# Kernel tuning notes

Measured on AMD Instinct MI355X. Metric: run time of the kernel, lower is better.

## Reference

```python
import jax, jax.numpy as jnp
import numpy as np

L, H, Z, B, SRC, K = 2, 1024, 256, 128, 64, 48
IN = Z + 1 + H  # z_i (+) k (+) attn


def _init(key, shape, fan_in):
    return jax.random.normal(key, shape, jnp.float32) / np.sqrt(fan_in)


def setup_inputs() -> dict:
    key = jax.random.key(0)
    ks = jax.random.split(key, 24)
    inp = {
        "h0": jax.random.normal(ks[0], (L, B, H), jnp.float32),
        "c0": jax.random.normal(ks[1], (L, B, H), jnp.float32),
        "context": jax.random.normal(ks[2], (B, SRC, H), jnp.float32),
        "z_0": jax.random.normal(ks[3], (B, Z), jnp.float32),
        "k": jax.random.randint(ks[4], (B, 1), 1, K + 1, jnp.int32),
        "eps": jax.random.normal(ks[5], (K, B, Z), jnp.float32),
        # StackedLSTM layer 0 (input IN) and layer 1 (input H)
        "W_ih0": _init(ks[6], (4 * H, IN), IN), "W_hh0": _init(ks[7], (4 * H, H), H),
        "b_ih0": jnp.zeros((4 * H,), jnp.float32), "b_hh0": jnp.zeros((4 * H,), jnp.float32),
        "W_ih1": _init(ks[8], (4 * H, H), H), "W_hh1": _init(ks[9], (4 * H, H), H),
        "b_ih1": jnp.zeros((4 * H,), jnp.float32), "b_hh1": jnp.zeros((4 * H,), jnp.float32),
        # GlobalAttentionLatent (Luong general)
        "attn_W_in": _init(ks[10], (H, H), H), "attn_W_out": _init(ks[11], (H, 2 * H), 2 * H),
        # GeneratorLatent
        "mu_W": _init(ks[12], (Z, H), H), "mu_b": jnp.zeros((Z,), jnp.float32),
        "sigma_W": _init(ks[13], (Z, H), H), "sigma_b": jnp.zeros((Z,), jnp.float32),
    }
    return inp


def _lstm_cell(x, h, c, W_ih, W_hh, b_ih, b_hh):
    gates = x @ W_ih.T + b_ih + h @ W_hh.T + b_hh
    i, f, g, o = jnp.split(gates, 4, axis=1)
    c_new = jax.nn.sigmoid(f) * c + jax.nn.sigmoid(i) * jnp.tanh(g)
    h_new = jax.nn.sigmoid(o) * jnp.tanh(c_new)
    return h_new, c_new


def _attend(q, context, W_in, W_out):
    # q: [B,H], context: [B,S,H] -> [B,H]
    scores = jnp.einsum('bsh,bh->bs', context, q @ W_in.T)
    align = jax.nn.softmax(scores, axis=1)
    weighted = jnp.einsum('bs,bsh->bh', align, context)
    return jnp.tanh(jnp.concatenate([weighted, q], axis=1) @ W_out.T)


def _forward(h0, c0, context, z_0, k, eps,
             W_ih0, W_hh0, b_ih0, b_hh0, W_ih1, W_hh1, b_ih1, b_hh1,
             attn_W_in, attn_W_out, mu_W, mu_b, sigma_W, sigma_b):
    k_max = eps.shape[0]
    k_f = k.astype(jnp.float32)  # [B,1]
    attn0 = _attend(c0[-1], context, attn_W_in, attn_W_out)

    def step(carry, inp):
        z_i, attn_o, h, c = carry
        i, eps_i = inp
        x = jnp.concatenate([z_i, k_f, attn_o], axis=1)  # [B, Z+1+H]
        h0n, c0n = _lstm_cell(x, h[0], c[0], W_ih0, W_hh0, b_ih0, b_hh0)
        h1n, c1n = _lstm_cell(h0n, h[1], c[1], W_ih1, W_hh1, b_ih1, b_hh1)
        h_new = jnp.stack([h0n, h1n])
        c_new = jnp.stack([c0n, c1n])
        frozen = (i >= k_f).astype(h_new.dtype)[None]  # [1,B,1]
        h_new = frozen * h + (1.0 - frozen) * h_new
        c_new = frozen * c + (1.0 - frozen) * c_new
        output = h1n  # rnn output before freezing, as in torch
        mu_i = output @ mu_W.T + mu_b
        sig_i = output @ sigma_W.T + sigma_b
        z_next = mu_i + jnp.exp(sig_i) * eps_i
        attn_new = _attend(output, context, attn_W_in, attn_W_out)
        return (z_next, attn_new, h_new, c_new), (z_next, mu_i, sig_i)

    steps = jnp.arange(k_max, dtype=jnp.float32)
    (_, _, h_f, c_f), (z, mu, sigma) = jax.lax.scan(
        step, (z_0, attn0, h0, c0), (steps, eps))
    valid = (steps[:, None] < k_f[:, 0][None, :])[:, :, None]  # [K,B,1]
    z = jnp.where(valid, z, 0.0)
    mu = jnp.where(valid, mu, 0.0)
    sigma = jnp.where(valid, sigma, 0.0)
    return (z.transpose(1, 0, 2), mu.transpose(1, 0, 2), sigma.transpose(1, 0, 2), h_f, c_f)


def reference(h0, c0, context, z_0, k, eps,
              W_ih0, W_hh0, b_ih0, b_hh0, W_ih1, W_hh1, b_ih1, b_hh1,
              attn_W_in, attn_W_out, mu_W, mu_b, sigma_W, sigma_b):
    return _forward(h0, c0, context, z_0, k, eps,
                    W_ih0, W_hh0, b_ih0, b_hh0, W_ih1, W_hh1, b_ih1, b_hh1,
                    attn_W_in, attn_W_out, mu_W, mu_b, sigma_W, sigma_b)
```

## Files before the change

kernel.cpp:

```cpp
#include <hip/hip_runtime.h>
#include <hip/hip_bf16.h>

#define L_ 2
#define H_ 1024
#define Z_ 256
#define B_ 128
#define SRC_ 64
#define K_ 48
#define BH_ (B_ * H_)
#define BZ_ (B_ * Z_)
#define BKZ_ ((size_t)B_ * K_ * Z_)
#define KA_ 2304
#define KB_ 2048

typedef unsigned short u16;
typedef __attribute__((ext_vector_type(8))) short short8;
typedef __attribute__((ext_vector_type(4))) float f32x4;

__device__ __align__(16) u16 g_Wc0[4096 * KA_];
__device__ __align__(16) u16 g_Wc1[4096 * KB_];
__device__ __align__(16) u16 g_Wmq[512 * 1024];
__device__ __align__(16) u16 g_Woutb[1024 * 2048];
__device__ __align__(16) u16 g_WinT[1024 * 1024];
__device__ __align__(16) u16 g_ctxb[8192 * 1024];
__device__ __align__(16) u16 g_ctxW[8192 * 1024];
__device__ __align__(16) u16 g_ctxWin[8192 * 1024];
__device__ __align__(16) u16 g_XA[2][B_ * KA_];
__device__ __align__(16) u16 g_XB[2][B_ * KB_];
__device__ __align__(16) u16 g_XC[B_ * H_];
__device__ float g_pb0[4096], g_pb1[4096], g_pbmq[512], g_wk0[4096];
__device__ float g_cs0[BH_], g_cs1[BH_], g_align[B_ * SRC_];
__device__ float g_cred[B_ * H_];
__device__ int g_perm[B_], g_inv[B_], g_kr[B_], g_Mact[K_];

__device__ __forceinline__ float sigm(float x) { return 1.0f / (1.0f + expf(-x)); }
__device__ __forceinline__ u16 f2b(float f) {
    union { float f; unsigned u; } x; x.f = f;
    unsigned r = x.u + 0x7fffu + ((x.u >> 16) & 1u);
    return (u16)(r >> 16);
}
__device__ __forceinline__ float b2f(u16 s) {
    union { unsigned u; float f; } x; x.u = ((unsigned)s) << 16;
    return x.f;
}

__global__ void k_sort(const int* __restrict__ kvec) {
    __shared__ int ks[B_];
    int t = threadIdx.x;
    if (t < B_) ks[t] = kvec[t];
    __syncthreads();
    if (t < B_) {
        int kb = ks[t], rank = 0;
        for (int j = 0; j < B_; ++j) { int kj = ks[j]; rank += (kj > kb) || (kj == kb && j < t); }
        g_perm[rank] = t; g_inv[t] = rank; g_kr[rank] = kb;
    }
    if (t < K_) { int c = 0; for (int j = 0; j < B_; ++j) c += (ks[j] > t); g_Mact[t] = c; }
}

__global__ void k_zero(float* __restrict__ out) {
    size_t n = 3 * BKZ_;
    for (size_t i = (size_t)blockIdx.x * 256 + threadIdx.x; i < n; i += (size_t)gridDim.x * 256)
        out[i] = 0.f;
}

__global__ void prep_wc0(const float* __restrict__ Wih, const float* __restrict__ Whh,
                         const float* __restrict__ bih, const float* __restrict__ bhh) {
    int n = blockIdx.x;
    int h = n >> 2, g = n & 3, r = g * 1024 + h;
    u16* row = g_Wc0 + (size_t)n * KA_;
    for (int j = threadIdx.x; j < KA_; j += 256) {
        float v = (j < 256) ? Wih[(size_t)r * 1281 + j]
                : (j < 1280) ? Wih[(size_t)r * 1281 + j + 1]
                             : Whh[(size_t)r * 1024 + (j - 1280)];
        row[j] = f2b(v);
    }
    if (threadIdx.x == 0) {
        g_wk0[n] = Wih[(size_t)r * 1281 + 256];
        g_pb0[n] = bih[r] + bhh[r];
    }
}

__global__ void prep_wc1(const float* __restrict__ Wih, const float* __restrict__ Whh,
                         const float* __restrict__ bih, const float* __restrict__ bhh) {
    int n = blockIdx.x;
    int h = n >> 2, g = n & 3, r = g * 1024 + h;
    u16* row = g_Wc1 + (size_t)n * KB_;
    for (int j = threadIdx.x; j < KB_; j += 256) {
        float v = (j < 1024) ? Wih[(size_t)r * 1024 + j] : Whh[(size_t)r * 1024 + (j - 1024)];
        row[j] = f2b(v);
    }
    if (threadIdx.x == 0) g_pb1[n] = bih[r] + bhh[r];
}

__global__ void prep_wmq(const float* __restrict__ muW, const float* __restrict__ mub,
                         const float* __restrict__ sgW, const float* __restrict__ sgb) {
    int n = blockIdx.x;
    int z = n >> 1, sel = n & 1;
    const float* src = sel ? sgW : muW;
    u16* row = g_Wmq + (size_t)n * 1024;
    for (int j = threadIdx.x; j < 1024; j += 256) row[j] = f2b(src[(size_t)z * 1024 + j]);
    if (threadIdx.x == 0) g_pbmq[n] = sel ? sgb[z] : mub[z];
}

__global__ void prep_copy(const float* __restrict__ in, u16* __restrict__ out, int n) {
    for (int i = blockIdx.x * 256 + threadIdx.x; i < n; i += gridDim.x * 256)
        out[i] = f2b(in[i]);
}

__global__ void prep_winT(const float* __restrict__ Win) {
    __shared__ float t[32][33];
    int bx = blockIdx.x * 32, by = blockIdx.y * 32;
    int tx = threadIdx.x & 31, ty0 = threadIdx.x >> 5;
    for (int it = 0; it < 4; ++it) {
        int ty = ty0 + it * 8;
        t[ty][tx] = Win[(size_t)(by + ty) * 1024 + bx + tx];
    }
    __syncthreads();
    for (int it = 0; it < 4; ++it) {
        int ty = ty0 + it * 8;
        g_WinT[(size_t)(bx + ty) * 1024 + by + tx] = f2b(t[tx][ty]);
    }
}

template <int K>
__device__ __forceinline__ void mmq(const u16* __restrict__ A, int sA,
                                    const u16* __restrict__ W, int sW,
                                    int m0, int n0, int w, int lane, f32x4& acc) {
    constexpr int KQ = K / 4;
    const int quad = lane >> 4, l16 = lane & 15;
    const u16* pa = A + (size_t)(m0 + l16) * sA + w * KQ + quad * 8;
    const u16* pw = W + (size_t)(n0 + l16) * sW + w * KQ + quad * 8;
#pragma unroll 4
    for (int k0 = 0; k0 < KQ; k0 += 32) {
        short8 a = *(const short8*)(const void*)(pa + k0);
        short8 b = *(const short8*)(const void*)(pw + k0);
        acc = __builtin_amdgcn_mfma_f32_16x16x32_bf16(a, b, acc, 0, 0, 0);
    }
}

__device__ __forceinline__ void stage_q(float* sm, int w, int lane, const f32x4& acc) {
    int quad = lane >> 4, l16 = lane & 15;
#pragma unroll
    for (int r = 0; r < 4; ++r) sm[w * 272 + (quad * 4 + r) * 17 + l16] = acc[r];
}

template <int K>
__device__ __forceinline__ void mm32(const u16* __restrict__ A, int sA,
                                     const u16* __restrict__ W, int sW,
                                     int m0, int n0, int w, int lane, f32x4 acc[2][2]) {
    constexpr int KQ = K / 4;
    const int quad = lane >> 4, l16 = lane & 15;
    const u16* pa0 = A + (size_t)(m0 + l16) * sA + w * KQ + quad * 8;
    const u16* pa1 = pa0 + (size_t)16 * sA;
    const u16* pb0 = W + (size_t)(n0 + l16) * sW + w * KQ + quad * 8;
    const u16* pb1 = pb0 + (size_t)16 * sW;
#pragma unroll 2
    for (int k0 = 0; k0 < KQ; k0 += 32) {
        short8 a0 = *(const short8*)(const void*)(pa0 + k0);
        short8 a1 = *(const short8*)(const void*)(pa1 + k0);
        short8 b0 = *(const short8*)(const void*)(pb0 + k0);
        short8 b1 = *(const short8*)(const void*)(pb1 + k0);
        acc[0][0] = __builtin_amdgcn_mfma_f32_16x16x32_bf16(a0, b0, acc[0][0], 0, 0, 0);
        acc[0][1] = __builtin_amdgcn_mfma_f32_16x16x32_bf16(a0, b1, acc[0][1], 0, 0, 0);
        acc[1][0] = __builtin_amdgcn_mfma_f32_16x16x32_bf16(a1, b0, acc[1][0], 0, 0, 0);
        acc[1][1] = __builtin_amdgcn_mfma_f32_16x16x32_bf16(a1, b1, acc[1][1], 0, 0, 0);
    }
}

template <int LAYER>
__global__ __launch_bounds__(256) void k_lstm(int step) {
    constexpr int K = (LAYER == 0) ? KA_ : KB_;
    const int p = step & 1;
    const u16* A = (LAYER == 0) ? g_XA[p] : g_XB[p];
    const u16* W = (LAYER == 0) ? g_Wc0 : g_Wc1;
    const float* pb = (LAYER == 0) ? g_pb0 : g_pb1;
    float* cs = (LAYER == 0) ? g_cs0 : g_cs1;
    const u16* stOld = (LAYER == 0) ? (g_XA[p] + 1280) : (g_XB[p] + 1024);
    u16* stNew = (LAYER == 0) ? (g_XA[1 - p] + 1280) : (g_XB[1 - p] + 1024);
    u16* hout = (LAYER == 0) ? g_XB[p] : g_XC;
    const int hoStride = (LAYER == 0) ? KB_ : 1024;

    const int tid = threadIdx.x, w = tid >> 6, lane = tid & 63;
    const int xcd = blockIdx.x & 7, loc = blockIdx.x >> 3;
    const int mt = loc & 3, nl = loc >> 2;
    const int m0 = mt * 32;
    const int n0 = (xcd * 16 + nl) * 32;
    const int Mact = g_Mact[step];

    if (m0 >= Mact) {
        const int r = m0 + (tid & 31), hg = (n0 >> 2) + (tid >> 5);
        stNew[(size_t)r * K + hg] = stOld[(size_t)r * K + hg];
        return;
    }

    __shared__ float smf[4 * 32 * 33];
    f32x4 acc[2][2] = {};
    mm32<K>(A, K, W, K, m0, n0, w, lane, acc);
    const int quad = lane >> 4, l16 = lane & 15;
#pragma unroll
    for (int i = 0; i < 2; ++i)
#pragma unroll
        for (int j = 0; j < 2; ++j)
#pragma unroll
            for (int r = 0; r < 4; ++r)
                smf[(w * 32 + i * 16 + quad * 4 + r) * 33 + j * 16 + l16] = acc[i][j][r];
    __syncthreads();
    const int bl = tid & 31, hl = tid >> 5;
    const int r = m0 + bl;
    float g[4];
#pragma unroll
    for (int gg = 0; gg < 4; ++gg) {
        int c = hl * 4 + gg;
        float s = smf[bl * 33 + c] + smf[(32 + bl) * 33 + c] +
                  smf[(64 + bl) * 33 + c] + smf[(96 + bl) * 33 + c];
        g[gg] = s + pb[n0 + c];
    }
    const int kr = g_kr[r];
    if (LAYER == 0) {
        float kf = (float)kr;
#pragma unroll
        for (int gg = 0; gg < 4; ++gg) g[gg] += kf * g_wk0[n0 + hl * 4 + gg];
    }
    const int hg = (n0 >> 2) + hl;
    float cold = cs[r * 1024 + hg];
    float cn = sigm(g[1]) * cold + sigm(g[0]) * tanhf(g[2]);
    float hn = sigm(g[3]) * tanhf(cn);
    hout[(size_t)r * hoStride + hg] = f2b(hn);
    if (step < kr) {
        stNew[(size_t)r * K + hg] = f2b(hn);
        cs[r * 1024 + hg] = cn;
    } else {
        stNew[(size_t)r * K + hg] = stOld[(size_t)r * K + hg];
    }
}

__global__ __launch_bounds__(256) void k_mix(const float* __restrict__ eps,
                                             float* __restrict__ out, int step,
                                             int do_mu, int do_sc) {
    __shared__ float sm[1344];
    const int tid = threadIdx.x;
    const int Mact = g_Mact[step];
    if (blockIdx.x < 256) {
        if (!do_mu) return;
        const int w = tid >> 6, lane = tid & 63;
        const int xcd = blockIdx.x & 7, loc = blockIdx.x >> 3;
        const int mt = loc & 7, nl = loc >> 3;
        const int m0 = mt * 16;
        const int n0 = (xcd * 4 + nl) * 16;
        if (m0 >= Mact) return;
        f32x4 acc = {0.f, 0.f, 0.f, 0.f};
        mmq<1024>(g_XC, 1024, g_Wmq, 1024, m0, n0, w, lane, acc);
        stage_q(sm, w, lane, acc);
        __syncthreads();
        if (tid < 128) {
            int bl = tid & 15, zl = tid >> 4;
            int r = m0 + bl;
            int c0 = 2 * zl, c1 = 2 * zl + 1;
            float mu = sm[bl * 17 + c0] + sm[272 + bl * 17 + c0] +
                       sm[544 + bl * 17 + c0] + sm[816 + bl * 17 + c0] + g_pbmq[n0 + c0];
            float sg = sm[bl * 17 + c1] + sm[272 + bl * 17 + c1] +
                       sm[544 + bl * 17 + c1] + sm[816 + bl * 17 + c1] + g_pbmq[n0 + c1];
            int zg = (n0 >> 1) + zl;
            int b = g_perm[r];
            float e = eps[((size_t)step * B_ + b) * Z_ + zg];
            float zn = mu + expf(sg) * e;
            g_XA[(step + 1) & 1][(size_t)r * KA_ + zg] = f2b(zn);
            bool valid = step < g_kr[r];
            size_t o = ((size_t)b * K_ + step) * Z_ + zg;
            out[o] = valid ? zn : 0.f;
            out[BKZ_ + o] = valid ? mu : 0.f;
            out[2 * BKZ_ + o] = valid ? sg : 0.f;
        }
    } else if (blockIdx.x < 384) {
        if (!do_sc) return;
        const int r = blockIdx.x - 256;
        if (r >= Mact) return;
        float* qf = sm;
        float* parts = sm + 1024;
        for (int i = tid; i < 1024; i += 256) qf[i] = b2f(g_XC[r * 1024 + i]);
        __syncthreads();
        int s = tid >> 2, part = tid & 3;
        const int b = g_perm[r];
        const u16* row = g_ctxWin + ((size_t)(b * SRC_ + s)) * 1024 + part * 256;
        float pacc = 0.f;
        for (int j = 0; j < 256; j += 8) {
            short8 v = *(const short8*)(const void*)(row + j);
#pragma unroll
            for (int t = 0; t < 8; ++t) pacc += qf[part * 256 + j + t] * b2f(((u16*)&v)[t]);
        }
        parts[s * 4 + part] = pacc;
        __syncthreads();
        if (tid < 64) {
            float v = parts[tid * 4] + parts[tid * 4 + 1] + parts[tid * 4 + 2] + parts[tid * 4 + 3];
            float mx = v;
            for (int o = 32; o; o >>= 1) mx = fmaxf(mx, __shfl_xor(mx, o, 64));
            float e = expf(v - mx), sum = e;
            for (int o = 32; o; o >>= 1) sum += __shfl_xor(sum, o, 64);
            g_align[r * SRC_ + tid] = e / sum;
        }
    } else {
        if (!do_sc) return;
        const int w = tid >> 6, lane = tid & 63;
        const int t = blockIdx.x - 384;
        const int xcd = t & 7, loc = t >> 3;
        const int mt = loc & 7, nl = loc >> 3;
        const int m0 = mt * 16;
        const int n0 = (xcd * 8 + nl) * 16;
        if (m0 >= Mact) return;
        f32x4 acc = {0.f, 0.f, 0.f, 0.f};
        mmq<1024>(g_XC, 1024, g_Woutb + 1024, 2048, m0, n0, w, lane, acc);
        stage_q(sm, w, lane, acc);
        __syncthreads();
        int bl = tid >> 4, hc = tid & 15;
        float cred = sm[bl * 17 + hc] + sm[272 + bl * 17 + hc] +
                     sm[544 + bl * 17 + hc] + sm[816 + bl * 17 + hc];
        g_cred[(size_t)(m0 + bl) * 1024 + n0 + hc] = cred;
    }
}

__global__ __launch_bounds__(256) void k_contract(int dp, int step) {
    __shared__ float sm[16 * SRC_];
    const int tid = threadIdx.x;
    const int xcd = blockIdx.x & 7, loc = blockIdx.x >> 3;
    const int mt = loc & 7, nl = loc >> 3;
    const int m0 = mt * 16;
    const int n0 = (xcd * 8 + nl) * 16;
    if (m0 >= g_Mact[step]) return;
    for (int i = tid; i < 16 * SRC_; i += 256)
        sm[i] = g_align[(m0 + (i >> 6)) * SRC_ + (i & 63)];
    __syncthreads();
    int bl = tid >> 4, hc = tid & 15;
    int r = m0 + bl;
    const int b = g_perm[r];
    const u16* base = g_ctxW + ((size_t)b * SRC_) * 1024 + n0 + hc;
    float a = g_cred[(size_t)r * 1024 + n0 + hc];
#pragma unroll 8
    for (int s = 0; s < SRC_; ++s) a += sm[bl * 64 + s] * b2f(base[(size_t)s * 1024]);
    g_XA[dp][(size_t)r * KA_ + 256 + n0 + hc] = f2b(tanhf(a));
}

__global__ void k_init(const float* __restrict__ h0, const float* __restrict__ c0,
                       const float* __restrict__ z0) {
    int i = blockIdx.x * 256 + threadIdx.x;
    int b = i >> 10, h = i & 1023;
    int r = g_inv[b];
    g_XA[0][(size_t)r * KA_ + 1280 + h] = f2b(h0[i]);
    g_XB[0][(size_t)r * KB_ + 1024 + h] = f2b(h0[BH_ + i]);
    g_XC[r * 1024 + h] = f2b(c0[BH_ + i]);
    g_cs0[r * 1024 + h] = c0[i];
    g_cs1[r * 1024 + h] = c0[BH_ + i];
    if (i < BZ_) {
        int bb = i >> 8, z = i & 255;
        g_XA[0][(size_t)g_inv[bb] * KA_ + z] = f2b(z0[i]);
    }
}

__global__ void k_final(float* __restrict__ out) {
    int i = blockIdx.x * 256 + threadIdx.x;
    int b = i >> 10, h = i & 1023;
    int r = g_inv[b];
    float* hf = out + (size_t)3 * BKZ_;
    float* cf = hf + 2 * BH_;
    hf[i] = b2f(g_XA[0][(size_t)r * KA_ + 1280 + h]);
    hf[BH_ + i] = b2f(g_XB[0][(size_t)r * KB_ + 1024 + h]);
    cf[i] = g_cs0[r * 1024 + h];
    cf[BH_ + i] = g_cs1[r * 1024 + h];
}

__global__ __launch_bounds__(256) void k_gemm_prep(const u16* __restrict__ A, int sA,
                                                   const u16* __restrict__ W, int sW,
                                                   u16* __restrict__ Out, int sO) {
    const int tid = threadIdx.x, w = tid >> 6, lane = tid & 63;
    const int quad = lane >> 4, l16 = lane & 15;
    const int xcd = blockIdx.x & 7, loc = blockIdx.x >> 3;
    const int n0 = (xcd * 2 + (loc & 1)) * 64;
    const int mb = (loc >> 1) * 128 + w * 32;
    f32x4 acc[2][4] = {};
    const u16* pa0 = A + (size_t)(mb + l16) * sA + quad * 8;
    const u16* pa1 = pa0 + (size_t)16 * sA;
    const u16* pw = W + (size_t)(n0 + l16) * sW + quad * 8;
#pragma unroll 2
    for (int k0 = 0; k0 < 1024; k0 += 32) {
        short8 a0 = *(const short8*)(const void*)(pa0 + k0);
        short8 a1 = *(const short8*)(const void*)(pa1 + k0);
#pragma unroll
        for (int j = 0; j < 4; ++j) {
            short8 b = *(const short8*)(const void*)(pw + (size_t)j * 16 * sW + k0);
            acc[0][j] = __builtin_amdgcn_mfma_f32_16x16x32_bf16(a0, b, acc[0][j], 0, 0, 0);
            acc[1][j] = __builtin_amdgcn_mfma_f32_16x16x32_bf16(a1, b, acc[1][j], 0, 0, 0);
        }
    }
#pragma unroll
    for (int i = 0; i < 2; ++i)
#pragma unroll
        for (int j = 0; j < 4; ++j)
#pragma unroll
            for (int r = 0; r < 4; ++r)
                Out[(size_t)(mb + i * 16 + quad * 4 + r) * sO + n0 + j * 16 + l16] =
                    f2b(acc[i][j][r]);
}

extern "C" void kernel_launch(void* const* d_in, const int* in_sizes, int n_in,
                              void* d_out, int out_size, void* d_ws, size_t ws_size,
                              hipStream_t stream) {
    (void)in_sizes; (void)n_in; (void)out_size; (void)d_ws; (void)ws_size;
    const float* h0 = (const float*)d_in[0];
    const float* c0 = (const float*)d_in[1];
    const float* ctx = (const float*)d_in[2];
    const float* z0 = (const float*)d_in[3];
    const int* kvec = (const int*)d_in[4];
    const float* eps = (const float*)d_in[5];
    const float* Wih0 = (const float*)d_in[6];
    const float* Whh0 = (const float*)d_in[7];
    const float* bih0 = (const float*)d_in[8];
    const float* bhh0 = (const float*)d_in[9];
    const float* Wih1 = (const float*)d_in[10];
    const float* Whh1 = (const float*)d_in[11];
    const float* bih1 = (const float*)d_in[12];
    const float* bhh1 = (const float*)d_in[13];
    const float* Win = (const float*)d_in[14];
    const float* Wout = (const float*)d_in[15];
    const float* muW = (const float*)d_in[16];
    const float* mub = (const float*)d_in[17];
    const float* sgW = (const float*)d_in[18];
    const float* sgb = (const float*)d_in[19];
    float* out = (float*)d_out;

    dim3 blk(256);
    k_sort<<<1, 128, 0, stream>>>(kvec);
    k_zero<<<2048, blk, 0, stream>>>(out);
    prep_wc0<<<4096, blk, 0, stream>>>(Wih0, Whh0, bih0, bhh0);
    prep_wc1<<<4096, blk, 0, stream>>>(Wih1, Whh1, bih1, bhh1);
    prep_wmq<<<512, blk, 0, stream>>>(muW, mub, sgW, sgb);
    {
        u16* woutb; hipGetSymbolAddress((void**)&woutb, HIP_SYMBOL(g_Woutb));
        u16* ctxb; hipGetSymbolAddress((void**)&ctxb, HIP_SYMBOL(g_ctxb));
        u16* winT; hipGetSymbolAddress((void**)&winT, HIP_SYMBOL(g_WinT));
        u16* ctxW; hipGetSymbolAddress((void**)&ctxW, HIP_SYMBOL(g_ctxW));
        u16* ctxWin; hipGetSymbolAddress((void**)&ctxWin, HIP_SYMBOL(g_ctxWin));
        prep_copy<<<2048, blk, 0, stream>>>(Wout, woutb, 1024 * 2048);
        prep_copy<<<8192, blk, 0, stream>>>(ctx, ctxb, 8192 * 1024);
        prep_winT<<<dim3(32, 32), blk, 0, stream>>>(Win);
        k_gemm_prep<<<1024, blk, 0, stream>>>(ctxb, 1024, woutb, 2048, ctxW, 1024);
        k_gemm_prep<<<1024, blk, 0, stream>>>(ctxb, 1024, winT, 1024, ctxWin, 1024);
    }
    k_init<<<BH_ / 256, blk, 0, stream>>>(h0, c0, z0);
    k_mix<<<896, blk, 0, stream>>>(eps, out, 0, 0, 1);
    k_contract<<<512, blk, 0, stream>>>(0, 0);

    for (int i = 0; i < K_; ++i) {
        k_lstm<0><<<512, blk, 0, stream>>>(i);
        k_lstm<1><<<512, blk, 0, stream>>>(i);
        const int more = (i + 1 < K_) ? 1 : 0;
        k_mix<<<896, blk, 0, stream>>>(eps, out, i, 1, more);
        if (more) k_contract<<<512, blk, 0, stream>>>((i + 1) & 1, i);
    }
    k_final<<<BH_ / 256, blk, 0, stream>>>(out);
}
```

Measured before the change: 3.213 ms.

## Fuse per-step recurrent kernels into one persistent kernel with grid barriers

Replaces the roughly 190 per-step kernel launches (two LSTM layers, mix, contract) with a single persistent kernel of 1024 blocks that moves between phases through a hierarchical atomic grid barrier, with per-XCD counters feeding a global counter. The aim is to remove launch overhead and inter-kernel gaps across the 48 sequential steps. It also merges the two precompute GEMMs into one launch with smaller per-warp tiles and raises the unroll factor in the LSTM matmul loop. The change relies on all 1024 blocks being co-resident; if they are not, the barrier deadlocks. Idle blocks in phases that use fewer blocks also spin at the barrier.

```diff
diff --git a/kernel.cpp b/kernel.cpp
--- a/kernel.cpp
+++ b/kernel.cpp
@@ -12,6 +12,8 @@
 #define BKZ_ ((size_t)B_ * K_ * Z_)
 #define KA_ 2304
 #define KB_ 2048
+#define NBLK_ 1024
+#define GRP_ (NBLK_ / 8)
 
 typedef unsigned short u16;
 typedef __attribute__((ext_vector_type(8))) short short8;
@@ -33,6 +35,9 @@
 __device__ float g_cred[B_ * H_];
 __device__ int g_perm[B_], g_inv[B_], g_kr[B_], g_Mact[K_];
 
+__device__ __align__(128) unsigned g_bar_x[8][32];
+__device__ __align__(128) unsigned g_bar_g;
+
 __device__ __forceinline__ float sigm(float x) { return 1.0f / (1.0f + expf(-x)); }
 __device__ __forceinline__ u16 f2b(float f) {
     union { float f; unsigned u; } x; x.f = f;
@@ -42,6 +47,22 @@
 __device__ __forceinline__ float b2f(u16 s) {
     union { unsigned u; float f; } x; x.u = ((unsigned)s) << 16;
     return x.f;
+}
+
+__device__ __forceinline__ void gsync(int bid, int bar) {
+    __syncthreads();
+    if (threadIdx.x == 0) {
+        __builtin_amdgcn_fence(__ATOMIC_RELEASE, "agent");
+        unsigned v = __hip_atomic_fetch_add(&g_bar_x[bid & 7][0], 1u,
+                                            __ATOMIC_RELAXED, __HIP_MEMORY_SCOPE_AGENT);
+        if (v == (unsigned)(bar * GRP_ + (GRP_ - 1)))
+            __hip_atomic_fetch_add(&g_bar_g, 1u, __ATOMIC_RELAXED, __HIP_MEMORY_SCOPE_AGENT);
+        while (__hip_atomic_load(&g_bar_g, __ATOMIC_RELAXED, __HIP_MEMORY_SCOPE_AGENT)
+               < (unsigned)(bar * 8 + 8))
+            __builtin_amdgcn_s_sleep(8);
+        __builtin_amdgcn_fence(__ATOMIC_ACQUIRE, "agent");
+    }
+    __syncthreads();
 }
 
 __global__ void k_sort(const int* __restrict__ kvec) {
@@ -154,7 +175,7 @@
     const u16* pa1 = pa0 + (size_t)16 * sA;
     const u16* pb0 = W + (size_t)(n0 + l16) * sW + w * KQ + quad * 8;
     const u16* pb1 = pb0 + (size_t)16 * sW;
-#pragma unroll 2
+#pragma unroll 4
     for (int k0 = 0; k0 < KQ; k0 += 32) {
         short8 a0 = *(const short8*)(const void*)(pa0 + k0);
         short8 a1 = *(const short8*)(const void*)(pa1 + k0);
@@ -168,7 +189,9 @@
 }
 
 template <int LAYER>
-__global__ __launch_bounds__(256) void k_lstm(int step) {
+__device__ __forceinline__ void lstm_phase(int bid, int tid, int w, int lane,
+                                           float* smf, int step) {
+    if (bid >= 512) return;
     constexpr int K = (LAYER == 0) ? KA_ : KB_;
     const int p = step & 1;
     const u16* A = (LAYER == 0) ? g_XA[p] : g_XB[p];
@@ -180,8 +203,7 @@
     u16* hout = (LAYER == 0) ? g_XB[p] : g_XC;
     const int hoStride = (LAYER == 0) ? KB_ : 1024;
 
-    const int tid = threadIdx.x, w = tid >> 6, lane = tid & 63;
-    const int xcd = blockIdx.x & 7, loc = blockIdx.x >> 3;
+    const int xcd = bid & 7, loc = bid >> 3;
     const int mt = loc & 3, nl = loc >> 2;
     const int m0 = mt * 32;
     const int n0 = (xcd * 16 + nl) * 32;
@@ -193,7 +215,6 @@
         return;
     }
 
-    __shared__ float smf[4 * 32 * 33];
     f32x4 acc[2][2] = {};
     mm32<K>(A, K, W, K, m0, n0, w, lane, acc);
     const int quad = lane >> 4, l16 = lane & 15;
@@ -234,16 +255,14 @@
     }
 }
 
-__global__ __launch_bounds__(256) void k_mix(const float* __restrict__ eps,
-                                             float* __restrict__ out, int step,
-                                             int do_mu, int do_sc) {
-    __shared__ float sm[1344];
-    const int tid = threadIdx.x;
+__device__ __forceinline__ void mix_phase(int bid, int tid, int w, int lane, float* sm,
+                                          const float* __restrict__ eps,
+                                          float* __restrict__ out,
+                                          int step, bool musig, bool sc) {
     const int Mact = g_Mact[step];
-    if (blockIdx.x < 256) {
-        if (!do_mu) return;
-        const int w = tid >> 6, lane = tid & 63;
-        const int xcd = blockIdx.x & 7, loc = blockIdx.x >> 3;
+    if (bid < 256) {
+        if (!musig) return;
+        const int xcd = bid & 7, loc = bid >> 3;
         const int mt = loc & 7, nl = loc >> 3;
         const int m0 = mt * 16;
         const int n0 = (xcd * 4 + nl) * 16;
@@ -271,9 +290,9 @@
             out[BKZ_ + o] = valid ? mu : 0.f;
             out[2 * BKZ_ + o] = valid ? sg : 0.f;
         }
-    } else if (blockIdx.x < 384) {
-        if (!do_sc) return;
-        const int r = blockIdx.x - 256;
+    } else if (bid < 384) {
+        if (!sc) return;
+        const int r = bid - 256;
         if (r >= Mact) return;
         float* qf = sm;
         float* parts = sm + 1024;
@@ -298,10 +317,9 @@
             for (int o = 32; o; o >>= 1) sum += __shfl_xor(sum, o, 64);
             g_align[r * SRC_ + tid] = e / sum;
         }
-    } else {
-        if (!do_sc) return;
-        const int w = tid >> 6, lane = tid & 63;
-        const int t = blockIdx.x - 384;
+    } else if (bid < 896) {
+        if (!sc) return;
+        const int t = bid - 384;
         const int xcd = t & 7, loc = t >> 3;
         const int mt = loc & 7, nl = loc >> 3;
         const int m0 = mt * 16;
@@ -318,10 +336,9 @@
     }
 }
 
-__global__ __launch_bounds__(256) void k_contract(int dp, int step) {
-    __shared__ float sm[16 * SRC_];
-    const int tid = threadIdx.x;
-    const int xcd = blockIdx.x & 7, loc = blockIdx.x >> 3;
+__device__ __forceinline__ void contract_phase(int bid, int tid, float* sm, int dp, int step) {
+    if (bid >= 512) return;
+    const int xcd = bid & 7, loc = bid >> 3;
     const int mt = loc & 7, nl = loc >> 3;
     const int m0 = mt * 16;
     const int n0 = (xcd * 8 + nl) * 16;
@@ -339,6 +356,34 @@
     g_XA[dp][(size_t)r * KA_ + 256 + n0 + hc] = f2b(tanhf(a));
 }
 
+__global__ __launch_bounds__(256, 4) void k_persist(const float* __restrict__ eps,
+                                                    float* __restrict__ out) {
+    const int bid = blockIdx.x;
+    const int tid = threadIdx.x;
+    const int w = tid >> 6, lane = tid & 63;
+    __shared__ float smf[4 * 32 * 33];
+    int bar = 0;
+
+    mix_phase(bid, tid, w, lane, smf, eps, out, 0, false, true);
+    gsync(bid, bar); ++bar;
+    contract_phase(bid, tid, smf, 0, 0);
+    gsync(bid, bar); ++bar;
+
+    for (int i = 0; i < K_; ++i) {
+        lstm_phase<0>(bid, tid, w, lane, smf, i);
+        gsync(bid, bar); ++bar;
+        lstm_phase<1>(bid, tid, w, lane, smf, i);
+        gsync(bid, bar); ++bar;
+        const bool more = (i + 1) < K_;
+        mix_phase(bid, tid, w, lane, smf, eps, out, i, true, more);
+        if (more) {
+            gsync(bid, bar); ++bar;
+            contract_phase(bid, tid, smf, (i + 1) & 1, i);
+            gsync(bid, bar); ++bar;
+        }
+    }
+}
+
 __global__ void k_init(const float* __restrict__ h0, const float* __restrict__ c0,
                        const float* __restrict__ z0) {
     int i = blockIdx.x * 256 + threadIdx.x;
@@ -353,6 +398,10 @@
         int bb = i >> 8, z = i & 255;
         g_XA[0][(size_t)g_inv[bb] * KA_ + z] = f2b(z0[i]);
     }
+    if (blockIdx.x == 0 && threadIdx.x == 0) {
+        g_bar_g = 0;
+        for (int x = 0; x < 8; ++x) g_bar_x[x][0] = 0;
+    }
 }
 
 __global__ void k_final(float* __restrict__ out) {
@@ -367,36 +416,45 @@
     cf[BH_ + i] = g_cs1[r * 1024 + h];
 }
 
-__global__ __launch_bounds__(256) void k_gemm_prep(const u16* __restrict__ A, int sA,
-                                                   const u16* __restrict__ W, int sW,
-                                                   u16* __restrict__ Out, int sO) {
+__global__ __launch_bounds__(256) void k_prep2(const u16* __restrict__ A,
+                                               const u16* __restrict__ W0,
+                                               const u16* __restrict__ W1,
+                                               u16* __restrict__ O0,
+                                               u16* __restrict__ O1) {
     const int tid = threadIdx.x, w = tid >> 6, lane = tid & 63;
     const int quad = lane >> 4, l16 = lane & 15;
+    const int wm = w >> 1, wn = w & 1;
     const int xcd = blockIdx.x & 7, loc = blockIdx.x >> 3;
-    const int n0 = (xcd * 2 + (loc & 1)) * 64;
-    const int mb = (loc >> 1) * 128 + w * 32;
-    f32x4 acc[2][4] = {};
-    const u16* pa0 = A + (size_t)(mb + l16) * sA + quad * 8;
-    const u16* pa1 = pa0 + (size_t)16 * sA;
-    const u16* pw = W + (size_t)(n0 + l16) * sW + quad * 8;
-#pragma unroll 2
+    const int nsub = loc & 3, mt = loc >> 2;
+    const bool sel = nsub >= 2;
+    const u16* W = sel ? W1 : W0;
+    const int sW = sel ? 1024 : 2048;
+    u16* Out = sel ? O1 : O0;
+    const int n0 = (xcd * 2 + (nsub & 1)) * 64 + wn * 32;
+    const int mb = mt * 64 + wm * 32;
+    f32x4 acc[2][2] = {};
+    const u16* pa0 = A + (size_t)(mb + l16) * 1024 + quad * 8;
+    const u16* pa1 = pa0 + (size_t)16 * 1024;
+    const u16* pb0 = W + (size_t)(n0 + l16) * sW + quad * 8;
+    const u16* pb1 = pb0 + (size_t)16 * sW;
+#pragma unroll 4
     for (int k0 = 0; k0 < 1024; k0 += 32) {
         short8 a0 = *(const short8*)(const void*)(pa0 + k0);
         short8 a1 = *(const short8*)(const void*)(pa1 + k0);
-#pragma unroll
-        for (int j = 0; j < 4; ++j) {
-            short8 b = *(const short8*)(const void*)(pw + (size_t)j * 16 * sW + k0);
-            acc[0][j] = __builtin_amdgcn_mfma_f32_16x16x32_bf16(a0, b, acc[0][j], 0, 0, 0);
-            acc[1][j] = __builtin_amdgcn_mfma_f32_16x16x32_bf16(a1, b, acc[1][j], 0, 0, 0);
-        }
+        short8 b0 = *(const short8*)(const void*)(pb0 + k0);
+        short8 b1 = *(const short8*)(const void*)(pb1 + k0);
+        acc[0][0] = __builtin_amdgcn_mfma_f32_16x16x32_bf16(a0, b0, acc[0][0], 0, 0, 0);
+        acc[0][1] = __builtin_amdgcn_mfma_f32_16x16x32_bf16(a0, b1, acc[0][1], 0, 0, 0);
+        acc[1][0] = __builtin_amdgcn_mfma_f32_16x16x32_bf16(a1, b0, acc[1][0], 0, 0, 0);
+        acc[1][1] = __builtin_amdgcn_mfma_f32_16x16x32_bf16(a1, b1, acc[1][1], 0, 0, 0);
     }
 #pragma unroll
     for (int i = 0; i < 2; ++i)
 #pragma unroll
-        for (int j = 0; j < 4; ++j)
+        for (int j = 0; j < 2; ++j)
 #pragma unroll
             for (int r = 0; r < 4; ++r)
-                Out[(size_t)(mb + i * 16 + quad * 4 + r) * sO + n0 + j * 16 + l16] =
+                Out[(size_t)(mb + i * 16 + quad * 4 + r) * 1024 + n0 + j * 16 + l16] =
                     f2b(acc[i][j][r]);
 }
 
@@ -441,19 +499,9 @@
         prep_copy<<<2048, blk, 0, stream>>>(Wout, woutb, 1024 * 2048);
         prep_copy<<<8192, blk, 0, stream>>>(ctx, ctxb, 8192 * 1024);
         prep_winT<<<dim3(32, 32), blk, 0, stream>>>(Win);
-        k_gemm_prep<<<1024, blk, 0, stream>>>(ctxb, 1024, woutb, 2048, ctxW, 1024);
-        k_gemm_prep<<<1024, blk, 0, stream>>>(ctxb, 1024, winT, 1024, ctxWin, 1024);
+        k_prep2<<<4096, blk, 0, stream>>>(ctxb, woutb, winT, ctxW, ctxWin);
     }
     k_init<<<BH_ / 256, blk, 0, stream>>>(h0, c0, z0);
-    k_mix<<<896, blk, 0, stream>>>(eps, out, 0, 0, 1);
-    k_contract<<<512, blk, 0, stream>>>(0, 0);
-
-    for (int i = 0; i < K_; ++i) {
-        k_lstm<0><<<512, blk, 0, stream>>>(i);
-        k_lstm<1><<<512, blk, 0, stream>>>(i);
-        const int more = (i + 1 < K_) ? 1 : 0;
-        k_mix<<<896, blk, 0, stream>>>(eps, out, i, 1, more);
-        if (more) k_contract<<<512, blk, 0, stream>>>((i + 1) & 1, i);
-    }
+    k_persist<<<NBLK_, blk, 0, stream>>>(eps, out);
     k_final<<<BH_ / 256, blk, 0, stream>>>(out);
 }
```

After: 9.096 ms. 183% more time.

## Fuse per-step kernels into one persistent kernel with custom grid barrier

Applied to the files above, without the earlier changes.

Replaces the roughly 190 per-step kernel launches of the recurrent loop with a single persistent kernel of 1024 blocks. The kernel runs the LSTM, mix and contract phases in sequence, separated by a software grid barrier built on flag arrays and cache-bypassing loads and stores. Double-buffered state arrays are expanded to one buffer per step, so no phase ever overwrites data that another phase might still read. It also raises the unroll factor of the inner MFMA loop. The aim is to remove launch overhead and inter-kernel gaps, at the cost of spin-wait barriers and a reliance on all 1024 blocks being co-resident, which risks deadlock otherwise.

```diff
diff --git a/kernel.cpp b/kernel.cpp
--- a/kernel.cpp
+++ b/kernel.cpp
@@ -7,15 +7,18 @@
 #define B_ 128
 #define SRC_ 64
 #define K_ 48
+#define NSTEP_ (K_ + 1)
 #define BH_ (B_ * H_)
 #define BZ_ (B_ * Z_)
 #define BKZ_ ((size_t)B_ * K_ * Z_)
 #define KA_ 2304
 #define KB_ 2048
+#define NBLK_ 1024
 
 typedef unsigned short u16;
 typedef __attribute__((ext_vector_type(8))) short short8;
 typedef __attribute__((ext_vector_type(4))) float f32x4;
+typedef __attribute__((ext_vector_type(4))) unsigned u32x4;
 
 __device__ __align__(16) u16 g_Wc0[4096 * KA_];
 __device__ __align__(16) u16 g_Wc1[4096 * KB_];
@@ -25,13 +28,17 @@
 __device__ __align__(16) u16 g_ctxb[8192 * 1024];
 __device__ __align__(16) u16 g_ctxW[8192 * 1024];
 __device__ __align__(16) u16 g_ctxWin[8192 * 1024];
-__device__ __align__(16) u16 g_XA[2][B_ * KA_];
-__device__ __align__(16) u16 g_XB[2][B_ * KB_];
-__device__ __align__(16) u16 g_XC[B_ * H_];
+__device__ __align__(16) u16 g_XA[NSTEP_][B_ * KA_];
+__device__ __align__(16) u16 g_XB[NSTEP_][B_ * KB_];
+__device__ __align__(16) u16 g_XC[NSTEP_][B_ * H_];
+__device__ float g_align[NSTEP_][B_ * SRC_];
+__device__ float g_cred[NSTEP_][B_ * H_];
 __device__ float g_pb0[4096], g_pb1[4096], g_pbmq[512], g_wk0[4096];
-__device__ float g_cs0[BH_], g_cs1[BH_], g_align[B_ * SRC_];
-__device__ float g_cred[B_ * H_];
+__device__ float g_cs0[BH_], g_cs1[BH_];
 __device__ int g_perm[B_], g_inv[B_], g_kr[B_], g_Mact[K_];
+
+__device__ unsigned g_flagv[NBLK_];
+__device__ __align__(128) unsigned g_done;
 
 __device__ __forceinline__ float sigm(float x) { return 1.0f / (1.0f + expf(-x)); }
 __device__ __forceinline__ u16 f2b(float f) {
@@ -42,6 +49,62 @@
 __device__ __forceinline__ float b2f(u16 s) {
     union { unsigned u; float f; } x; x.u = ((unsigned)s) << 16;
     return x.f;
+}
+__device__ __forceinline__ unsigned umin2(unsigned a, unsigned b) { return a < b ? a : b; }
+
+__device__ __forceinline__ void st16_llc(u16* p, u16 v) {
+    unsigned vv = v;
+    asm volatile("global_store_short %0, %1, off sc0 sc1" :: "v"(p), "v"(vv) : "memory");
+}
+__device__ __forceinline__ void st32_llc(float* p, float v) {
+    asm volatile("global_store_dword %0, %1, off sc0 sc1" :: "v"(p), "v"(v) : "memory");
+}
+__device__ __forceinline__ void st32u_llc(unsigned* p, unsigned v) {
+    asm volatile("global_store_dword %0, %1, off sc0 sc1" :: "v"(p), "v"(v) : "memory");
+}
+__device__ __forceinline__ unsigned ld32u_llc(const unsigned* p) {
+    unsigned r;
+    asm volatile("global_load_dword %0, %1, off sc0 sc1\n\ts_waitcnt vmcnt(0)"
+                 : "=v"(r) : "v"(p) : "memory");
+    return r;
+}
+__device__ __forceinline__ unsigned min16_llc(const unsigned* p) {
+    u32x4 a, b, c, d;
+    asm volatile("global_load_dwordx4 %0, %4, off sc0 sc1\n\t"
+                 "global_load_dwordx4 %1, %4, off offset:16 sc0 sc1\n\t"
+                 "global_load_dwordx4 %2, %4, off offset:32 sc0 sc1\n\t"
+                 "global_load_dwordx4 %3, %4, off offset:48 sc0 sc1\n\t"
+                 "s_waitcnt vmcnt(0)"
+                 : "=v"(a), "=v"(b), "=v"(c), "=v"(d) : "v"(p) : "memory");
+    unsigned m0 = umin2(umin2(a[0], a[1]), umin2(a[2], a[3]));
+    unsigned m1 = umin2(umin2(b[0], b[1]), umin2(b[2], b[3]));
+    unsigned m2 = umin2(umin2(c[0], c[1]), umin2(c[2], c[3]));
+    unsigned m3 = umin2(umin2(d[0], d[1]), umin2(d[2], d[3]));
+    return umin2(umin2(m0, m1), umin2(m2, m3));
+}
+
+__device__ __forceinline__ void gsync(int bid, int tid, unsigned bar) {
+    asm volatile("s_waitcnt vmcnt(0)" ::: "memory");
+    __syncthreads();
+    if (bid == NBLK_ - 1) {
+        if (tid < 64) {
+            if (tid == 0) st32u_llc(&g_flagv[bid], bar);
+            const unsigned* p = g_flagv + tid * 16;
+            for (;;) {
+                unsigned m = min16_llc(p);
+                if (__all((int)(m >= bar))) break;
+                __builtin_amdgcn_s_sleep(2);
+            }
+            if (tid == 0) st32u_llc(&g_done, bar);
+        }
+        __syncthreads();
+    } else {
+        if (tid == 0) {
+            st32u_llc(&g_flagv[bid], bar);
+            while (ld32u_llc(&g_done) < bar) __builtin_amdgcn_s_sleep(4);
+        }
+        __syncthreads();
+    }
 }
 
 __global__ void k_sort(const int* __restrict__ kvec) {
@@ -154,7 +217,7 @@
     const u16* pa1 = pa0 + (size_t)16 * sA;
     const u16* pb0 = W + (size_t)(n0 + l16) * sW + w * KQ + quad * 8;
     const u16* pb1 = pb0 + (size_t)16 * sW;
-#pragma unroll 2
+#pragma unroll 4
     for (int k0 = 0; k0 < KQ; k0 += 32) {
         short8 a0 = *(const short8*)(const void*)(pa0 + k0);
         short8 a1 = *(const short8*)(const void*)(pa1 + k0);
@@ -168,20 +231,20 @@
 }
 
 template <int LAYER>
-__global__ __launch_bounds__(256) void k_lstm(int step) {
+__device__ __forceinline__ void lstm_phase(int bid, int tid, int w, int lane,
+                                           float* smf, int step) {
+    if (bid >= 512) return;
     constexpr int K = (LAYER == 0) ? KA_ : KB_;
-    const int p = step & 1;
-    const u16* A = (LAYER == 0) ? g_XA[p] : g_XB[p];
-    const u16* W = (LAYER == 0) ? g_Wc0 : g_Wc1;
+    const u16* A = (LAYER == 0) ? g_XA[step] : g_XB[step];
+    const u16* Wt = (LAYER == 0) ? g_Wc0 : g_Wc1;
     const float* pb = (LAYER == 0) ? g_pb0 : g_pb1;
     float* cs = (LAYER == 0) ? g_cs0 : g_cs1;
-    const u16* stOld = (LAYER == 0) ? (g_XA[p] + 1280) : (g_XB[p] + 1024);
-    u16* stNew = (LAYER == 0) ? (g_XA[1 - p] + 1280) : (g_XB[1 - p] + 1024);
-    u16* hout = (LAYER == 0) ? g_XB[p] : g_XC;
+    const u16* stOld = (LAYER == 0) ? (g_XA[step] + 1280) : (g_XB[step] + 1024);
+    u16* stNew = (LAYER == 0) ? (g_XA[step + 1] + 1280) : (g_XB[step + 1] + 1024);
+    u16* hout = (LAYER == 0) ? g_XB[step] : g_XC[step + 1];
     const int hoStride = (LAYER == 0) ? KB_ : 1024;
 
-    const int tid = threadIdx.x, w = tid >> 6, lane = tid & 63;
-    const int xcd = blockIdx.x & 7, loc = blockIdx.x >> 3;
+    const int xcd = bid & 7, loc = bid >> 3;
     const int mt = loc & 3, nl = loc >> 2;
     const int m0 = mt * 32;
     const int n0 = (xcd * 16 + nl) * 32;
@@ -189,13 +252,12 @@
 
     if (m0 >= Mact) {
         const int r = m0 + (tid & 31), hg = (n0 >> 2) + (tid >> 5);
-        stNew[(size_t)r * K + hg] = stOld[(size_t)r * K + hg];
+        st16_llc(&stNew[(size_t)r * K + hg], stOld[(size_t)r * K + hg]);
         return;
     }
 
-    __shared__ float smf[4 * 32 * 33];
     f32x4 acc[2][2] = {};
-    mm32<K>(A, K, W, K, m0, n0, w, lane, acc);
+    mm32<K>(A, K, Wt, K, m0, n0, w, lane, acc);
     const int quad = lane >> 4, l16 = lane & 15;
 #pragma unroll
     for (int i = 0; i < 2; ++i)
@@ -225,31 +287,29 @@
     float cold = cs[r * 1024 + hg];
     float cn = sigm(g[1]) * cold + sigm(g[0]) * tanhf(g[2]);
     float hn = sigm(g[3]) * tanhf(cn);
-    hout[(size_t)r * hoStride + hg] = f2b(hn);
+    st16_llc(&hout[(size_t)r * hoStride + hg], f2b(hn));
     if (step < kr) {
-        stNew[(size_t)r * K + hg] = f2b(hn);
+        st16_llc(&stNew[(size_t)r * K + hg], f2b(hn));
         cs[r * 1024 + hg] = cn;
     } else {
-        stNew[(size_t)r * K + hg] = stOld[(size_t)r * K + hg];
-    }
-}
-
-__global__ __launch_bounds__(256) void k_mix(const float* __restrict__ eps,
-                                             float* __restrict__ out, int step,
-                                             int do_mu, int do_sc) {
-    __shared__ float sm[1344];
-    const int tid = threadIdx.x;
+        st16_llc(&stNew[(size_t)r * K + hg], stOld[(size_t)r * K + hg]);
+    }
+}
+
+__device__ __forceinline__ void mix_phase(int bid, int tid, int w, int lane, float* sm,
+                                          const float* __restrict__ eps,
+                                          float* __restrict__ out,
+                                          int qi, int step, bool musig, bool sc) {
     const int Mact = g_Mact[step];
-    if (blockIdx.x < 256) {
-        if (!do_mu) return;
-        const int w = tid >> 6, lane = tid & 63;
-        const int xcd = blockIdx.x & 7, loc = blockIdx.x >> 3;
+    if (bid < 256) {
+        if (!musig) return;
+        const int xcd = bid & 7, loc = bid >> 3;
         const int mt = loc & 7, nl = loc >> 3;
         const int m0 = mt * 16;
         const int n0 = (xcd * 4 + nl) * 16;
         if (m0 >= Mact) return;
         f32x4 acc = {0.f, 0.f, 0.f, 0.f};
-        mmq<1024>(g_XC, 1024, g_Wmq, 1024, m0, n0, w, lane, acc);
+        mmq<1024>(g_XC[qi], 1024, g_Wmq, 1024, m0, n0, w, lane, acc);
         stage_q(sm, w, lane, acc);
         __syncthreads();
         if (tid < 128) {
@@ -264,20 +324,20 @@
             int b = g_perm[r];
             float e = eps[((size_t)step * B_ + b) * Z_ + zg];
             float zn = mu + expf(sg) * e;
-            g_XA[(step + 1) & 1][(size_t)r * KA_ + zg] = f2b(zn);
+            st16_llc(&g_XA[qi][(size_t)r * KA_ + zg], f2b(zn));
             bool valid = step < g_kr[r];
             size_t o = ((size_t)b * K_ + step) * Z_ + zg;
             out[o] = valid ? zn : 0.f;
             out[BKZ_ + o] = valid ? mu : 0.f;
             out[2 * BKZ_ + o] = valid ? sg : 0.f;
         }
-    } else if (blockIdx.x < 384) {
-        if (!do_sc) return;
-        const int r = blockIdx.x - 256;
+    } else if (bid < 384) {
+        if (!sc) return;
+        const int r = bid - 256;
         if (r >= Mact) return;
         float* qf = sm;
         float* parts = sm + 1024;
-        for (int i = tid; i < 1024; i += 256) qf[i] = b2f(g_XC[r * 1024 + i]);
+        for (int i = tid; i < 1024; i += 256) qf[i] = b2f(g_XC[qi][r * 1024 + i]);
         __syncthreads();
         int s = tid >> 2, part = tid & 3;
         const int b = g_perm[r];
@@ -296,47 +356,73 @@
             for (int o = 32; o; o >>= 1) mx = fmaxf(mx, __shfl_xor(mx, o, 64));
             float e = expf(v - mx), sum = e;
             for (int o = 32; o; o >>= 1) sum += __shfl_xor(sum, o, 64);
-            g_align[r * SRC_ + tid] = e / sum;
-        }
-    } else {
-        if (!do_sc) return;
-        const int w = tid >> 6, lane = tid & 63;
-        const int t = blockIdx.x - 384;
+            st32_llc(&g_align[qi][r * SRC_ + tid], e / sum);
+        }
+    } else if (bid < 896) {
+        if (!sc) return;
+        const int t = bid - 384;
         const int xcd = t & 7, loc = t >> 3;
         const int mt = loc & 7, nl = loc >> 3;
         const int m0 = mt * 16;
         const int n0 = (xcd * 8 + nl) * 16;
         if (m0 >= Mact) return;
         f32x4 acc = {0.f, 0.f, 0.f, 0.f};
-        mmq<1024>(g_XC, 1024, g_Woutb + 1024, 2048, m0, n0, w, lane, acc);
+        mmq<1024>(g_XC[qi], 1024, g_Woutb + 1024, 2048, m0, n0, w, lane, acc);
         stage_q(sm, w, lane, acc);
         __syncthreads();
         int bl = tid >> 4, hc = tid & 15;
         float cred = sm[bl * 17 + hc] + sm[272 + bl * 17 + hc] +
                      sm[544 + bl * 17 + hc] + sm[816 + bl * 17 + hc];
-        g_cred[(size_t)(m0 + bl) * 1024 + n0 + hc] = cred;
-    }
-}
-
-__global__ __launch_bounds__(256) void k_contract(int dp, int step) {
-    __shared__ float sm[16 * SRC_];
-    const int tid = threadIdx.x;
-    const int xcd = blockIdx.x & 7, loc = blockIdx.x >> 3;
+        st32_llc(&g_cred[qi][(size_t)(m0 + bl) * 1024 + n0 + hc], cred);
+    }
+}
+
+__device__ __forceinline__ void contract_phase(int bid, int tid, float* sm, int qi, int step) {
+    if (bid >= 512) return;
+    const int xcd = bid & 7, loc = bid >> 3;
     const int mt = loc & 7, nl = loc >> 3;
     const int m0 = mt * 16;
     const int n0 = (xcd * 8 + nl) * 16;
     if (m0 >= g_Mact[step]) return;
     for (int i = tid; i < 16 * SRC_; i += 256)
-        sm[i] = g_align[(m0 + (i >> 6)) * SRC_ + (i & 63)];
+        sm[i] = g_align[qi][(m0 + (i >> 6)) * SRC_ + (i & 63)];
     __syncthreads();
     int bl = tid >> 4, hc = tid & 15;
     int r = m0 + bl;
     const int b = g_perm[r];
     const u16* base = g_ctxW + ((size_t)b * SRC_) * 1024 + n0 + hc;
-    float a = g_cred[(size_t)r * 1024 + n0 + hc];
+    float a = g_cred[qi][(size_t)r * 1024 + n0 + hc];
 #pragma unroll 8
     for (int s = 0; s < SRC_; ++s) a += sm[bl * 64 + s] * b2f(base[(size_t)s * 1024]);
-    g_XA[dp][(size_t)r * KA_ + 256 + n0 + hc] = f2b(tanhf(a));
+    st16_llc(&g_XA[qi][(size_t)r * KA_ + 256 + n0 + hc], f2b(tanhf(a)));
+}
+
+__global__ __launch_bounds__(256, 4) void k_persist(const float* __restrict__ eps,
+                                                    float* __restrict__ out) {
+    const int bid = blockIdx.x;
+    const int tid = threadIdx.x;
+    const int w = tid >> 6, lane = tid & 63;
+    __shared__ float smf[4 * 32 * 33];
+    unsigned bar = 0;
+
+    mix_phase(bid, tid, w, lane, smf, eps, out, 0, 0, false, true);
+    gsync(bid, tid, ++bar);
+    contract_phase(bid, tid, smf, 0, 0);
+    gsync(bid, tid, ++bar);
+
+    for (int i = 0; i < K_; ++i) {
+        lstm_phase<0>(bid, tid, w, lane, smf, i);
+        gsync(bid, tid, ++bar);
+        lstm_phase<1>(bid, tid, w, lane, smf, i);
+        gsync(bid, tid, ++bar);
+        const bool more = (i + 1) < K_;
+        mix_phase(bid, tid, w, lane, smf, eps, out, i + 1, i, true, more);
+        if (more) {
+            gsync(bid, tid, ++bar);
+            contract_phase(bid, tid, smf, i + 1, i);
+            gsync(bid, tid, ++bar);
+        }
+    }
 }
 
 __global__ void k_init(const float* __restrict__ h0, const float* __restrict__ c0,
@@ -346,13 +432,15 @@
     int r = g_inv[b];
     g_XA[0][(size_t)r * KA_ + 1280 + h] = f2b(h0[i]);
     g_XB[0][(size_t)r * KB_ + 1024 + h] = f2b(h0[BH_ + i]);
-    g_XC[r * 1024 + h] = f2b(c0[BH_ + i]);
+    g_XC[0][r * 1024 + h] = f2b(c0[BH_ + i]);
     g_cs0[r * 1024 + h] = c0[i];
     g_cs1[r * 1024 + h] = c0[BH_ + i];
     if (i < BZ_) {
         int bb = i >> 8, z = i & 255;
         g_XA[0][(size_t)g_inv[bb] * KA_ + z] = f2b(z0[i]);
     }
+    if (i < NBLK_) g_flagv[i] = 0;
+    if (i == 0) g_done = 0;
 }
 
 __global__ void k_final(float* __restrict__ out) {
@@ -361,8 +449,8 @@
     int r = g_inv[b];
     float* hf = out + (size_t)3 * BKZ_;
     float* cf = hf + 2 * BH_;
-    hf[i] = b2f(g_XA[0][(size_t)r * KA_ + 1280 + h]);
-    hf[BH_ + i] = b2f(g_XB[0][(size_t)r * KB_ + 1024 + h]);
+    hf[i] = b2f(g_XA[K_][(size_t)r * KA_ + 1280 + h]);
+    hf[BH_ + i] = b2f(g_XB[K_][(size_t)r * KB_ + 1024 + h]);
     cf[i] = g_cs0[r * 1024 + h];
     cf[BH_ + i] = g_cs1[r * 1024 + h];
 }
@@ -445,15 +533,6 @@
         k_gemm_prep<<<1024, blk, 0, stream>>>(ctxb, 1024, winT, 1024, ctxWin, 1024);
     }
     k_init<<<BH_ / 256, blk, 0, stream>>>(h0, c0, z0);
-    k_mix<<<896, blk, 0, stream>>>(eps, out, 0, 0, 1);
-    k_contract<<<512, blk, 0, stream>>>(0, 0);
-
-    for (int i = 0; i < K_; ++i) {
-        k_lstm<0><<<512, blk, 0, stream>>>(i);
-        k_lstm<1><<<512, blk, 0, stream>>>(i);
-        const int more = (i + 1 < K_) ? 1 : 0;
-        k_mix<<<896, blk, 0, stream>>>(eps, out, i, 1, more);
-        if (more) k_contract<<<512, blk, 0, stream>>>((i + 1) & 1, i);
-    }
+    k_persist<<<NBLK_, blk, 0, stream>>>(eps, out);
     k_final<<<BH_ / 256, blk, 0, stream>>>(out);
 }
```

Measured after the change: 4.318 ms. 34.4% more time.
